# Kernel tuning notes

Measured on AMD Instinct MI355X. Metric: run time of the kernel, lower is better.

The kernel has to match this reference:

```python
import jax, jax.numpy as jnp
import numpy as np


def setup_inputs() -> dict:
    key = jax.random.key(0)
    k1, k2, k3 = jax.random.split(key, 3)
    B, C, T = 8, 16, 131072
    O, n_keep, n_discard = 16, 48, 16
    x = jax.random.normal(k1, (B, C, T), dtype=jnp.float32)
    weight = jax.random.normal(k2, (O, C * n_keep), dtype=jnp.float32) * 0.05
    bias = jax.random.normal(k3, (O,), dtype=jnp.float32) * 0.05
    return {"x": x, "weight": weight, "bias": bias,
            "n_discard": n_discard, "n_keep": n_keep}


def reference(x, weight, bias, n_discard, n_keep):
    # x: (B, C, T); weight: (O, C*n_keep); bias: (O,)
    B, C, T = x.shape
    O = weight.shape[0]
    S = n_keep + n_discard              # window (group) size
    G = -(-T // S)                      # number of groups
    pad = G * S - T
    xp = jnp.pad(x, ((0, 0), (0, 0), (0, pad)))
    # per-timestep weight blocks: (n_keep, C, O), zero-padded for discarded frames -> (S, C, O)
    w = weight.reshape(O, C, n_keep).transpose(2, 1, 0)
    w = jnp.pad(w, ((n_discard, 0), (0, 0), (0, 0)))
    # group the time axis: (B, C, G, S)
    xg = xp.reshape(B, C, G, S)
    # per-timestep projection then causal cumsum within each window
    y = jnp.einsum('bcgs,sco->bgso', xg, w)   # (B, G, S, O)
    y = jnp.cumsum(y, axis=2) + bias          # reset every window; bias seeds each window
    y = y.transpose(0, 3, 1, 2).reshape(B, O, G * S)
    return y[..., :T]
```

## Files before the change

### kernel.cpp

```cpp
#include <hip/hip_runtime.h>


#define CC 16
#define TT 131072
#define OO 16
#define NK 48
#define ND 16
#define WPB 4
#define GG 2048

#define SCAN_STEP(CTRL, RMASK)                                                  \
  {                                                                             \
    int t_ = __builtin_amdgcn_update_dpp(0, __float_as_int(v), (CTRL), (RMASK), \
                                         0xf, true);                            \
    v += __int_as_float(t_);                                                    \
  }

__device__ __forceinline__ float wave_scan64(float v) {
  SCAN_STEP(0x111, 0xf)
  SCAN_STEP(0x112, 0xf)
  SCAN_STEP(0x114, 0xf)
  SCAN_STEP(0x118, 0xf)
  SCAN_STEP(0x142, 0xa)
  SCAN_STEP(0x143, 0xc)
  return v;
}

__global__ __launch_bounds__(256, 4) void cfl_kernel(
    const float* __restrict__ x, const float* __restrict__ weight,
    const float* __restrict__ bias, float* __restrict__ out) {
  __shared__ __attribute__((aligned(16))) float tile[4 * 256 * 4];

  const int tid = threadIdx.x;
  const int lane = tid & 63;
  const int wid = tid >> 6;

  const int n0 = blockIdx.x * WPB;
  const int b = n0 >> 11;
  const int t0 = (n0 & (GG - 1)) * 64;

  const float* xb = x + (size_t)b * CC * TT + t0;
  {
    const int sw = (tid >> 3) & 3;
#pragma unroll
    for (int c = 0; c < CC; ++c) {
      float v = xb[(size_t)c * TT + tid];
      tile[(((c >> 2) * 256 + tid) << 2) + ((c & 3) ^ sw)] = v;
    }
  }
  __syncthreads();

  float* ob = out + (size_t)b * OO * TT + t0;
  const int perm = (lane >> 3) & 3;

#pragma unroll
  for (int p = 0; p < 2; ++p) {
    const int o0 = p * 4 + wid;

    float w0p[CC], w1p[CC];
#pragma unroll
    for (int c4 = 0; c4 < 4; ++c4) {
#pragma unroll
      for (int j = 0; j < 4; ++j) {
        const int ce = c4 * 4 + (j ^ perm);
        float a = 0.f, bq = 0.f;
        if (lane >= ND) {
          a = weight[o0 * (CC * NK) + ce * NK + (lane - ND)];
          bq = weight[(o0 + 8) * (CC * NK) + ce * NK + (lane - ND)];
        }
        w0p[c4 * 4 + j] = a;
        w1p[c4 * 4 + j] = bq;
      }
    }
    const float b0 = bias[o0];
    const float b1 = bias[o0 + 8];

#pragma unroll
    for (int k = 0; k < WPB; ++k) {
      const int t = k * 64 + lane;
      const float4 xq0 = *(const float4*)&tile[(0 * 256 + t) << 2];
      const float4 xq1 = *(const float4*)&tile[(1 * 256 + t) << 2];
      const float4 xq2 = *(const float4*)&tile[(2 * 256 + t) << 2];
      const float4 xq3 = *(const float4*)&tile[(3 * 256 + t) << 2];

      float p0 = 0.f, p1 = 0.f;
      p0 = fmaf(xq0.x, w0p[0], p0);  p1 = fmaf(xq0.x, w1p[0], p1);
      p0 = fmaf(xq0.y, w0p[1], p0);  p1 = fmaf(xq0.y, w1p[1], p1);
      p0 = fmaf(xq0.z, w0p[2], p0);  p1 = fmaf(xq0.z, w1p[2], p1);
      p0 = fmaf(xq0.w, w0p[3], p0);  p1 = fmaf(xq0.w, w1p[3], p1);
      p0 = fmaf(xq1.x, w0p[4], p0);  p1 = fmaf(xq1.x, w1p[4], p1);
      p0 = fmaf(xq1.y, w0p[5], p0);  p1 = fmaf(xq1.y, w1p[5], p1);
      p0 = fmaf(xq1.z, w0p[6], p0);  p1 = fmaf(xq1.z, w1p[6], p1);
      p0 = fmaf(xq1.w, w0p[7], p0);  p1 = fmaf(xq1.w, w1p[7], p1);
      p0 = fmaf(xq2.x, w0p[8], p0);  p1 = fmaf(xq2.x, w1p[8], p1);
      p0 = fmaf(xq2.y, w0p[9], p0);  p1 = fmaf(xq2.y, w1p[9], p1);
      p0 = fmaf(xq2.z, w0p[10], p0); p1 = fmaf(xq2.z, w1p[10], p1);
      p0 = fmaf(xq2.w, w0p[11], p0); p1 = fmaf(xq2.w, w1p[11], p1);
      p0 = fmaf(xq3.x, w0p[12], p0); p1 = fmaf(xq3.x, w1p[12], p1);
      p0 = fmaf(xq3.y, w0p[13], p0); p1 = fmaf(xq3.y, w1p[13], p1);
      p0 = fmaf(xq3.z, w0p[14], p0); p1 = fmaf(xq3.z, w1p[14], p1);
      p0 = fmaf(xq3.w, w0p[15], p0); p1 = fmaf(xq3.w, w1p[15], p1);

      const float cs0 = wave_scan64(p0);
      const float cs1 = wave_scan64(p1);
      ob[(size_t)o0 * TT + t] = cs0 + b0;
      ob[(size_t)(o0 + 8) * TT + t] = cs1 + b1;
    }
  }
}

extern "C" void kernel_launch(void* const* d_in, const int* in_sizes, int n_in,
                              void* d_out, int out_size, void* d_ws, size_t ws_size,
                              hipStream_t stream) {
  const float* x = (const float*)d_in[0];
  const float* weight = (const float*)d_in[1];
  const float* bias = (const float*)d_in[2];
  float* out = (float*)d_out;

  cfl_kernel<<<4096, 256, 0, stream>>>(x, weight, bias, out);
}
```

Before: 33.78 us.

## Enlarge blocks to 16 windows with 8 waves, load weights once per wave

Each block now handles 1024 timesteps (16 windows) with 512 threads. Each of the 8 waves owns one output pair (o, o+8) for all windows, so weights are loaded into registers once instead of twice per block, and the loads overlap the x staging before the barrier. The x tile grows to 64KB of LDS and is loaded in two batches of 16 independent global loads to raise memory-level parallelism. In exchange, the much larger LDS footprint and fewer blocks lower occupancy, and each block has a longer serial compute tail after the load phase.

```diff
diff --git a/kernel.cpp b/kernel.cpp
--- a/kernel.cpp
+++ b/kernel.cpp
@@ -6,8 +6,9 @@
 #define OO 16
 #define NK 48
 #define ND 16
-#define WPB 4
 #define GG 2048
+#define NWIN 16
+#define NTILE 4
 
 #define SCAN_STEP(CTRL, RMASK)                                                  \
   {                                                                             \
@@ -26,86 +27,99 @@
   return v;
 }
 
-__global__ __launch_bounds__(256, 4) void cfl_kernel(
+__global__ __launch_bounds__(512, 4) void cfl_kernel(
     const float* __restrict__ x, const float* __restrict__ weight,
     const float* __restrict__ bias, float* __restrict__ out) {
-  __shared__ __attribute__((aligned(16))) float tile[4 * 256 * 4];
+  __shared__ __attribute__((aligned(16))) float xt[NTILE * 4 * 256 * 4];
 
   const int tid = threadIdx.x;
   const int lane = tid & 63;
   const int wid = tid >> 6;
 
-  const int n0 = blockIdx.x * WPB;
-  const int b = n0 >> 11;
-  const int t0 = (n0 & (GG - 1)) * 64;
+  const int blk = blockIdx.x;
+  const int b = blk >> 7;
+  const int t00 = (blk & 127) * (NWIN * 64);
 
-  const float* xb = x + (size_t)b * CC * TT + t0;
-  {
-    const int sw = (tid >> 3) & 3;
+  const float* xb = x + (size_t)b * CC * TT + t00;
+
 #pragma unroll
-    for (int c = 0; c < CC; ++c) {
-      float v = xb[(size_t)c * TT + tid];
-      tile[(((c >> 2) * 256 + tid) << 2) + ((c & 3) ^ sw)] = v;
+  for (int batch = 0; batch < 2; ++batch) {
+    float xs[16];
+#pragma unroll
+    for (int i = 0; i < 16; ++i) {
+      const int c = batch * 8 + (i >> 1);
+      const int sub = i & 1;
+      xs[i] = xb[(size_t)c * TT + sub * 512 + tid];
+    }
+#pragma unroll
+    for (int i = 0; i < 16; ++i) asm volatile("" : "+v"(xs[i]));
+#pragma unroll
+    for (int i = 0; i < 16; ++i) {
+      const int c = batch * 8 + (i >> 1);
+      const int t = (i & 1) * 512 + tid;
+      const int tt = t >> 8;
+      const int tl = t & 255;
+      const int slot = (c & 3) ^ ((tl >> 3) & 3);
+      xt[(((tt * 4 + (c >> 2)) * 256 + tl) << 2) + slot] = xs[i];
     }
   }
+
+  const int o0 = wid, o1 = wid + 8;
+  const int perm = (lane >> 3) & 3;
+  float w0p[CC], w1p[CC];
+#pragma unroll
+  for (int c4 = 0; c4 < 4; ++c4) {
+#pragma unroll
+    for (int j = 0; j < 4; ++j) {
+      const int ce = c4 * 4 + (j ^ perm);
+      float a = 0.f, bq = 0.f;
+      if (lane >= ND) {
+        a = weight[o0 * (CC * NK) + ce * NK + (lane - ND)];
+        bq = weight[o1 * (CC * NK) + ce * NK + (lane - ND)];
+      }
+      asm volatile("" : "+v"(a), "+v"(bq));
+      w0p[c4 * 4 + j] = a;
+      w1p[c4 * 4 + j] = bq;
+    }
+  }
+  const float b0 = bias[o0];
+  const float b1 = bias[o1];
+
   __syncthreads();
 
-  float* ob = out + (size_t)b * OO * TT + t0;
-  const int perm = (lane >> 3) & 3;
+  float* ob = out + (size_t)b * OO * TT + t00;
 
 #pragma unroll
-  for (int p = 0; p < 2; ++p) {
-    const int o0 = p * 4 + wid;
+  for (int win = 0; win < NWIN; ++win) {
+    const int tt = win >> 2;
+    const int t = (win & 3) * 64 + lane;
+    const float4 xq0 = *(const float4*)&xt[(((tt * 4 + 0) * 256 + t) << 2)];
+    const float4 xq1 = *(const float4*)&xt[(((tt * 4 + 1) * 256 + t) << 2)];
+    const float4 xq2 = *(const float4*)&xt[(((tt * 4 + 2) * 256 + t) << 2)];
+    const float4 xq3 = *(const float4*)&xt[(((tt * 4 + 3) * 256 + t) << 2)];
 
-    float w0p[CC], w1p[CC];
-#pragma unroll
-    for (int c4 = 0; c4 < 4; ++c4) {
-#pragma unroll
-      for (int j = 0; j < 4; ++j) {
-        const int ce = c4 * 4 + (j ^ perm);
-        float a = 0.f, bq = 0.f;
-        if (lane >= ND) {
-          a = weight[o0 * (CC * NK) + ce * NK + (lane - ND)];
-          bq = weight[(o0 + 8) * (CC * NK) + ce * NK + (lane - ND)];
-        }
-        w0p[c4 * 4 + j] = a;
-        w1p[c4 * 4 + j] = bq;
-      }
-    }
-    const float b0 = bias[o0];
-    const float b1 = bias[o0 + 8];
+    float p0 = 0.f, p1 = 0.f;
+    p0 = fmaf(xq0.x, w0p[0], p0);  p1 = fmaf(xq0.x, w1p[0], p1);
+    p0 = fmaf(xq0.y, w0p[1], p0);  p1 = fmaf(xq0.y, w1p[1], p1);
+    p0 = fmaf(xq0.z, w0p[2], p0);  p1 = fmaf(xq0.z, w1p[2], p1);
+    p0 = fmaf(xq0.w, w0p[3], p0);  p1 = fmaf(xq0.w, w1p[3], p1);
+    p0 = fmaf(xq1.x, w0p[4], p0);  p1 = fmaf(xq1.x, w1p[4], p1);
+    p0 = fmaf(xq1.y, w0p[5], p0);  p1 = fmaf(xq1.y, w1p[5], p1);
+    p0 = fmaf(xq1.z, w0p[6], p0);  p1 = fmaf(xq1.z, w1p[6], p1);
+    p0 = fmaf(xq1.w, w0p[7], p0);  p1 = fmaf(xq1.w, w1p[7], p1);
+    p0 = fmaf(xq2.x, w0p[8], p0);  p1 = fmaf(xq2.x, w1p[8], p1);
+    p0 = fmaf(xq2.y, w0p[9], p0);  p1 = fmaf(xq2.y, w1p[9], p1);
+    p0 = fmaf(xq2.z, w0p[10], p0); p1 = fmaf(xq2.z, w1p[10], p1);
+    p0 = fmaf(xq2.w, w0p[11], p0); p1 = fmaf(xq2.w, w1p[11], p1);
+    p0 = fmaf(xq3.x, w0p[12], p0); p1 = fmaf(xq3.x, w1p[12], p1);
+    p0 = fmaf(xq3.y, w0p[13], p0); p1 = fmaf(xq3.y, w1p[13], p1);
+    p0 = fmaf(xq3.z, w0p[14], p0); p1 = fmaf(xq3.z, w1p[14], p1);
+    p0 = fmaf(xq3.w, w0p[15], p0); p1 = fmaf(xq3.w, w1p[15], p1);
 
-#pragma unroll
-    for (int k = 0; k < WPB; ++k) {
-      const int t = k * 64 + lane;
-      const float4 xq0 = *(const float4*)&tile[(0 * 256 + t) << 2];
-      const float4 xq1 = *(const float4*)&tile[(1 * 256 + t) << 2];
-      const float4 xq2 = *(const float4*)&tile[(2 * 256 + t) << 2];
-      const float4 xq3 = *(const float4*)&tile[(3 * 256 + t) << 2];
-
-      float p0 = 0.f, p1 = 0.f;
-      p0 = fmaf(xq0.x, w0p[0], p0);  p1 = fmaf(xq0.x, w1p[0], p1);
-      p0 = fmaf(xq0.y, w0p[1], p0);  p1 = fmaf(xq0.y, w1p[1], p1);
-      p0 = fmaf(xq0.z, w0p[2], p0);  p1 = fmaf(xq0.z, w1p[2], p1);
-      p0 = fmaf(xq0.w, w0p[3], p0);  p1 = fmaf(xq0.w, w1p[3], p1);
-      p0 = fmaf(xq1.x, w0p[4], p0);  p1 = fmaf(xq1.x, w1p[4], p1);
-      p0 = fmaf(xq1.y, w0p[5], p0);  p1 = fmaf(xq1.y, w1p[5], p1);
-      p0 = fmaf(xq1.z, w0p[6], p0);  p1 = fmaf(xq1.z, w1p[6], p1);
-      p0 = fmaf(xq1.w, w0p[7], p0);  p1 = fmaf(xq1.w, w1p[7], p1);
-      p0 = fmaf(xq2.x, w0p[8], p0);  p1 = fmaf(xq2.x, w1p[8], p1);
-      p0 = fmaf(xq2.y, w0p[9], p0);  p1 = fmaf(xq2.y, w1p[9], p1);
-      p0 = fmaf(xq2.z, w0p[10], p0); p1 = fmaf(xq2.z, w1p[10], p1);
-      p0 = fmaf(xq2.w, w0p[11], p0); p1 = fmaf(xq2.w, w1p[11], p1);
-      p0 = fmaf(xq3.x, w0p[12], p0); p1 = fmaf(xq3.x, w1p[12], p1);
-      p0 = fmaf(xq3.y, w0p[13], p0); p1 = fmaf(xq3.y, w1p[13], p1);
-      p0 = fmaf(xq3.z, w0p[14], p0); p1 = fmaf(xq3.z, w1p[14], p1);
-      p0 = fmaf(xq3.w, w0p[15], p0); p1 = fmaf(xq3.w, w1p[15], p1);
-
-      const float cs0 = wave_scan64(p0);
-      const float cs1 = wave_scan64(p1);
-      ob[(size_t)o0 * TT + t] = cs0 + b0;
-      ob[(size_t)(o0 + 8) * TT + t] = cs1 + b1;
-    }
+    const float cs0 = wave_scan64(p0) + b0;
+    const float cs1 = wave_scan64(p1) + b1;
+    ob[(size_t)o0 * TT + win * 64 + lane] = cs0;
+    ob[(size_t)o1 * TT + win * 64 + lane] = cs1;
   }
 }
 
@@ -117,5 +131,5 @@
   const float* bias = (const float*)d_in[2];
   float* out = (float*)d_out;
 
-  cfl_kernel<<<4096, 256, 0, stream>>>(x, weight, bias, out);
+  cfl_kernel<<<1024, 512, 0, stream>>>(x, weight, bias, out);
 }
```

Measured after the change: 36.22 us. 1.07x slower.
